# Performance work log

Measured on AMD Instinct MI355X. Metric: run time of the kernel, lower is better.

The kernel has to match this reference:

```python
import jax, jax.numpy as jnp
import numpy as np

B, T, D, H = 4, 4096, 1024, 16
HD = D // H  # head_dim = 64


def setup_inputs() -> dict:
    key = jax.random.key(0)
    k1, k2, k3 = jax.random.split(key, 3)
    x = jax.random.normal(k1, (B, T, D), dtype=jnp.float32)
    # torch Linear weight is (out,in); we store transposed (in,out) for x @ W
    Wqkv = jax.random.normal(k2, (D, 3 * D), dtype=jnp.float32) * 0.02
    Wout = jax.random.normal(k3, (D, D), dtype=jnp.float32) * 0.02
    return {"x": x, "Wqkv": Wqkv, "Wout": Wout}


def reference(x, Wqkv, Wout):
    # Faithful to original: qkv reshaped to (B,T,3,H,hd) WITHOUT moving heads to
    # a batch dim, so attention mixes the H heads of each token (scores: B,T,H,H).
    qkv = (x @ Wqkv).reshape(B, T, 3, H, HD)
    q, k, v = qkv[:, :, 0], qkv[:, :, 1], qkv[:, :, 2]  # each (B,T,H,HD)
    scores = jnp.einsum('btid,btjd->btij', q, k) / jnp.sqrt(jnp.float32(HD))
    attn = jax.nn.softmax(scores, axis=-1)  # softmax over heads j
    out = jnp.einsum('btij,btjd->btid', attn, v).reshape(B, T, D)
    return out @ Wout
```

## Files before the change

### kernel.cpp

```cpp
#include <hip/hip_runtime.h>
#include <hip/hip_bf16.h>
#include <cstdint>
#include <cstddef>


typedef __bf16 bf16x8 __attribute__((ext_vector_type(8)));
typedef __bf16 bf16x4 __attribute__((ext_vector_type(4)));
typedef float  f32x4  __attribute__((ext_vector_type(4)));

#define AS1 __attribute__((address_space(1)))
#define AS3 __attribute__((address_space(3)))

__device__ __forceinline__ void async_copy16(const void* g, void* l) {
    __builtin_amdgcn_global_load_lds((const AS1 void*)g, (AS3 void*)l, 16, 0, 0);
}

__global__ __launch_bounds__(256) void cvt_bf16_kernel(const float4* __restrict__ in,
                                                       bf16x4* __restrict__ out, int n4) {
    int i = blockIdx.x * 256 + threadIdx.x;
    if (i >= n4) return;
    float4 v = in[i];
    bf16x4 o = { (__bf16)v.x, (__bf16)v.y, (__bf16)v.z, (__bf16)v.w };
    out[i] = o;
}

__global__ __launch_bounds__(256) void transpose_cvt_kernel(const float* __restrict__ in,
                                                            __bf16* __restrict__ out,
                                                            int R, int C) {
    __shared__ float tile[32][33];
    int c0 = blockIdx.x * 32, r0 = blockIdx.y * 32;
    int tx = threadIdx.x, ty = threadIdx.y;
    #pragma unroll
    for (int i = 0; i < 32; i += 8)
        tile[ty + i][tx] = in[(size_t)(r0 + ty + i) * C + c0 + tx];
    __syncthreads();
    #pragma unroll
    for (int i = 0; i < 32; i += 8)
        out[(size_t)(c0 + ty + i) * R + r0 + tx] = (__bf16)tile[tx][ty + i];
}

template<int OUT_BF16>
__global__ __launch_bounds__(256) void gemm_bt(const __bf16* __restrict__ A,
                                               const __bf16* __restrict__ Bt,
                                               void* __restrict__ Cv,
                                               int N, int K) {
    __shared__ __bf16 As[128 * 32];
    __shared__ __bf16 Bs[128 * 32];

    const int tid  = threadIdx.x;
    const int wave = tid >> 6;
    const int lane = tid & 63;
    const int quad = lane >> 4;
    const int q16  = lane & 15;
    const int wr   = wave >> 1, wc = wave & 1;
    const int row0 = blockIdx.y * 128;
    const int col0 = blockIdx.x * 128;

    const __bf16* Ag = A  + (size_t)row0 * K;
    const __bf16* Bg = Bt + (size_t)col0 * K;

    const int o0 = (wave * 2)     * 1024 + lane * 16;
    const int o1 = (wave * 2 + 1) * 1024 + lane * 16;
    const int r0 = o0 >> 6, r1 = o1 >> 6;
    const int cb0 = ((o0 >> 4) & 3) ^ ((r0 >> 1) & 3);
    const int cb1 = ((o1 >> 4) & 3) ^ ((r1 >> 1) & 3);
    char* ldsA0 = (char*)As + (wave * 2)     * 1024;
    char* ldsA1 = (char*)As + (wave * 2 + 1) * 1024;
    char* ldsB0 = (char*)Bs + (wave * 2)     * 1024;
    char* ldsB1 = (char*)Bs + (wave * 2 + 1) * 1024;

    f32x4 acc[4][4] = {};

    for (int k0 = 0; k0 < K; k0 += 32) {
        async_copy16(Ag + (size_t)r0 * K + (k0 + cb0 * 8), ldsA0);
        async_copy16(Ag + (size_t)r1 * K + (k0 + cb1 * 8), ldsA1);
        async_copy16(Bg + (size_t)r0 * K + (k0 + cb0 * 8), ldsB0);
        async_copy16(Bg + (size_t)r1 * K + (k0 + cb1 * 8), ldsB1);
        __syncthreads();

        bf16x8 af[4], bfr[4];
        #pragma unroll
        for (int mi = 0; mi < 4; ++mi) {
            int row = wr * 64 + mi * 16 + q16;
            int sl  = quad ^ ((row >> 1) & 3);
            af[mi] = *(const bf16x8*)((const char*)As + row * 64 + sl * 16);
        }
        #pragma unroll
        for (int ni = 0; ni < 4; ++ni) {
            int row = wc * 64 + ni * 16 + q16;
            int sl  = quad ^ ((row >> 1) & 3);
            bfr[ni] = *(const bf16x8*)((const char*)Bs + row * 64 + sl * 16);
        }
        #pragma unroll
        for (int mi = 0; mi < 4; ++mi)
            #pragma unroll
            for (int ni = 0; ni < 4; ++ni)
                acc[mi][ni] = __builtin_amdgcn_mfma_f32_16x16x32_bf16(af[mi], bfr[ni], acc[mi][ni], 0, 0, 0);
        __syncthreads();
    }

    #pragma unroll
    for (int mi = 0; mi < 4; ++mi) {
        #pragma unroll
        for (int ni = 0; ni < 4; ++ni) {
            int col = col0 + wc * 64 + ni * 16 + q16;
            #pragma unroll
            for (int r = 0; r < 4; ++r) {
                int row = row0 + wr * 64 + mi * 16 + quad * 4 + r;
                if (OUT_BF16)
                    ((__bf16*)Cv)[(size_t)row * N + col] = (__bf16)acc[mi][ni][r];
                else
                    ((float*)Cv)[(size_t)row * N + col] = acc[mi][ni][r];
            }
        }
    }
}

__global__ __launch_bounds__(256) void attn_mfma_kernel(const __bf16* __restrict__ qkv,
                                                        __bf16* __restrict__ ao) {
    const int tok  = blockIdx.x * 4 + (threadIdx.x >> 6);
    const int lane = threadIdx.x & 63;
    const int quad = lane >> 4;
    const int q16  = lane & 15;

    const __bf16* base = qkv + (size_t)tok * 3072;
    const __bf16* vb   = base + 2048;

    const bf16x8 qf0 = *(const bf16x8*)(base + q16 * 64 + quad * 8);
    const bf16x8 qf1 = *(const bf16x8*)(base + q16 * 64 + quad * 8 + 32);
    const bf16x8 kf0 = *(const bf16x8*)(base + 1024 + q16 * 64 + quad * 8);
    const bf16x8 kf1 = *(const bf16x8*)(base + 1024 + q16 * 64 + quad * 8 + 32);

    f32x4 st = {0.f, 0.f, 0.f, 0.f};
    st = __builtin_amdgcn_mfma_f32_16x16x32_bf16(kf0, qf0, st, 0, 0, 0);
    st = __builtin_amdgcn_mfma_f32_16x16x32_bf16(kf1, qf1, st, 0, 0, 0);

    float s0 = st[0] * 0.125f, s1 = st[1] * 0.125f, s2 = st[2] * 0.125f, s3 = st[3] * 0.125f;
    float m = fmaxf(fmaxf(s0, s1), fmaxf(s2, s3));
    m = fmaxf(m, __shfl_xor(m, 16));
    m = fmaxf(m, __shfl_xor(m, 32));
    float e0 = __expf(s0 - m), e1 = __expf(s1 - m), e2 = __expf(s2 - m), e3 = __expf(s3 - m);
    float sum = e0 + e1 + e2 + e3;
    sum += __shfl_xor(sum, 16);
    sum += __shfl_xor(sum, 32);
    const float inv = 1.f / sum;

    union { __bf16 h[2]; int i; } u01, u23;
    u01.h[0] = (__bf16)(e0 * inv); u01.h[1] = (__bf16)(e1 * inv);
    u23.h[0] = (__bf16)(e2 * inv); u23.h[1] = (__bf16)(e3 * inv);

    const int src0 = quad * 32 + q16;
    const int src1 = src0 + 16;
    union { int i[4]; bf16x8 v; } af;
    af.i[0] = __shfl(u01.i, src0);
    af.i[1] = __shfl(u23.i, src0);
    af.i[2] = __shfl(u01.i, src1);
    af.i[3] = __shfl(u23.i, src1);
    if (quad >= 2) { af.i[0] = 0; af.i[1] = 0; af.i[2] = 0; af.i[3] = 0; }

    __bf16* outp = ao + (size_t)tok * 1024;
    #pragma unroll
    for (int c = 0; c < 4; ++c) {
        const int d0 = c * 16;
        bf16x8 bf = {};
        if (quad < 2) {
            #pragma unroll
            for (int idx = 0; idx < 8; ++idx)
                bf[idx] = vb[(quad * 8 + idx) * 64 + d0 + q16];
        }
        f32x4 acc = {0.f, 0.f, 0.f, 0.f};
        acc = __builtin_amdgcn_mfma_f32_16x16x32_bf16(af.v, bf, acc, 0, 0, 0);
        #pragma unroll
        for (int r = 0; r < 4; ++r)
            outp[(quad * 4 + r) * 64 + d0 + q16] = (__bf16)acc[r];
    }
}

extern "C" void kernel_launch(void* const* d_in, const int* in_sizes, int n_in,
                              void* d_out, int out_size, void* d_ws, size_t ws_size,
                              hipStream_t stream) {
    const float* x    = (const float*)d_in[0];
    const float* Wqkv = (const float*)d_in[1];
    const float* Wout = (const float*)d_in[2];
    float* out = (float*)d_out;

    char* ws = (char*)d_ws;
    __bf16* xb    = (__bf16*)(ws);
    __bf16* wqkvT = (__bf16*)(ws + 33554432);
    __bf16* woutT = (__bf16*)(ws + 33554432 + 6291456);
    __bf16* qkv   = (__bf16*)(ws + 33554432 + 6291456 + 2097152);
    __bf16* ao    = (__bf16*)(ws + 33554432 + 6291456 + 2097152 + 100663296);

    cvt_bf16_kernel<<<16384, 256, 0, stream>>>((const float4*)x, (bf16x4*)xb, 4194304);
    transpose_cvt_kernel<<<dim3(96, 32), dim3(32, 8), 0, stream>>>(Wqkv, wqkvT, 1024, 3072);
    transpose_cvt_kernel<<<dim3(32, 32), dim3(32, 8), 0, stream>>>(Wout, woutT, 1024, 1024);
    gemm_bt<1><<<dim3(24, 128), 256, 0, stream>>>(xb, wqkvT, (void*)qkv, 3072, 1024);
    attn_mfma_kernel<<<4096, 256, 0, stream>>>(qkv, ao);
    gemm_bt<0><<<dim3(8, 128), 256, 0, stream>>>(ao, woutT, (void*)out, 1024, 1024);
}
```

Before: 350.4 us.

## Permute weight columns so attention loads and stores are contiguous vectors

The transpose kernels now permute the output columns of Wqkv and the input rows of Wout, so the QKV GEMM writes q/k/v in the exact per-lane fragment order the attention MFMAs consume. The attention output is written in a permuted order that the permuted Wout rows undo. This turns strided scalar V gathers and scattered 2-byte output stores into 16-byte vector loads and stores. The attention kernel is a small part of the total compared with the two GEMMs, and the weight preprocessing gains index arithmetic and less coalesced scattered writes.

Result: no change. 350.3 us (-0.0%).

```diff
diff --git a/kernel.cpp b/kernel.cpp
--- a/kernel.cpp
+++ b/kernel.cpp
@@ -13,6 +13,17 @@
 
 __device__ __forceinline__ void async_copy16(const void* g, void* l) {
     __builtin_amdgcn_global_load_lds((const AS1 void*)g, (AS3 void*)l, 16, 0, 0);
+}
+
+__device__ __forceinline__ int invp_qkv(int col) {
+    int g = col >> 10;
+    if (g == 2) { int q = col & 1023; return 2048 + ((q & 63) << 4) + (q >> 6); }
+    int h = (col >> 6) & 15, d = col & 63;
+    return (g << 10) + ((d & 32) << 4) + (((d >> 3) & 3) << 7) + (h << 3) + (d & 7);
+}
+
+__device__ __forceinline__ int invp_ao(int k) {
+    return (((k >> 8) & 3) << 8) + ((k & 15) << 4) + (((k >> 4) & 3) << 2) + ((k >> 6) & 3);
 }
 
 __global__ __launch_bounds__(256) void cvt_bf16_kernel(const float4* __restrict__ in,
@@ -24,10 +35,10 @@
     out[i] = o;
 }
 
-__global__ __launch_bounds__(256) void transpose_cvt_kernel(const float* __restrict__ in,
-                                                            __bf16* __restrict__ out,
-                                                            int R, int C) {
+__global__ __launch_bounds__(256) void transpose_qkv_kernel(const float* __restrict__ in,
+                                                            __bf16* __restrict__ out) {
     __shared__ float tile[32][33];
+    const int C = 3072;
     int c0 = blockIdx.x * 32, r0 = blockIdx.y * 32;
     int tx = threadIdx.x, ty = threadIdx.y;
     #pragma unroll
@@ -35,8 +46,26 @@
         tile[ty + i][tx] = in[(size_t)(r0 + ty + i) * C + c0 + tx];
     __syncthreads();
     #pragma unroll
+    for (int i = 0; i < 32; i += 8) {
+        int prow = invp_qkv(c0 + ty + i);
+        out[(size_t)prow * 1024 + r0 + tx] = (__bf16)tile[tx][ty + i];
+    }
+}
+
+__global__ __launch_bounds__(256) void transpose_wout_kernel(const float* __restrict__ in,
+                                                             __bf16* __restrict__ out) {
+    __shared__ float tile[32][33];
+    const int C = 1024;
+    int c0 = blockIdx.x * 32, r0 = blockIdx.y * 32;
+    int tx = threadIdx.x, ty = threadIdx.y;
+    #pragma unroll
     for (int i = 0; i < 32; i += 8)
-        out[(size_t)(c0 + ty + i) * R + r0 + tx] = (__bf16)tile[tx][ty + i];
+        tile[ty + i][tx] = in[(size_t)(r0 + ty + i) * C + c0 + tx];
+    __syncthreads();
+    int pk = invp_ao(r0 + tx);
+    #pragma unroll
+    for (int i = 0; i < 32; i += 8)
+        out[(size_t)(c0 + ty + i) * 1024 + pk] = (__bf16)tile[tx][ty + i];
 }
 
 template<int OUT_BF16>
@@ -124,12 +153,11 @@
     const int q16  = lane & 15;
 
     const __bf16* base = qkv + (size_t)tok * 3072;
-    const __bf16* vb   = base + 2048;
-
-    const bf16x8 qf0 = *(const bf16x8*)(base + q16 * 64 + quad * 8);
-    const bf16x8 qf1 = *(const bf16x8*)(base + q16 * 64 + quad * 8 + 32);
-    const bf16x8 kf0 = *(const bf16x8*)(base + 1024 + q16 * 64 + quad * 8);
-    const bf16x8 kf1 = *(const bf16x8*)(base + 1024 + q16 * 64 + quad * 8 + 32);
+
+    const bf16x8 qf0 = *(const bf16x8*)(base + lane * 8);
+    const bf16x8 qf1 = *(const bf16x8*)(base + 512 + lane * 8);
+    const bf16x8 kf0 = *(const bf16x8*)(base + 1024 + lane * 8);
+    const bf16x8 kf1 = *(const bf16x8*)(base + 1536 + lane * 8);
 
     f32x4 st = {0.f, 0.f, 0.f, 0.f};
     st = __builtin_amdgcn_mfma_f32_16x16x32_bf16(kf0, qf0, st, 0, 0, 0);
@@ -158,22 +186,26 @@
     af.i[3] = __shfl(u23.i, src1);
     if (quad >= 2) { af.i[0] = 0; af.i[1] = 0; af.i[2] = 0; af.i[3] = 0; }
 
-    __bf16* outp = ao + (size_t)tok * 1024;
+    const __bf16* vb = base + 2048;
+    f32x4 accs[4];
     #pragma unroll
     for (int c = 0; c < 4; ++c) {
-        const int d0 = c * 16;
-        bf16x8 bf = {};
-        if (quad < 2) {
-            #pragma unroll
-            for (int idx = 0; idx < 8; ++idx)
-                bf[idx] = vb[(quad * 8 + idx) * 64 + d0 + q16];
-        }
-        f32x4 acc = {0.f, 0.f, 0.f, 0.f};
-        acc = __builtin_amdgcn_mfma_f32_16x16x32_bf16(af.v, bf, acc, 0, 0, 0);
+        bf16x8 bfv = {};
+        if (quad < 2)
+            bfv = *(const bf16x8*)(vb + (c * 16 + q16) * 16 + quad * 8);
+        f32x4 z = {0.f, 0.f, 0.f, 0.f};
+        accs[c] = __builtin_amdgcn_mfma_f32_16x16x32_bf16(af.v, bfv, z, 0, 0, 0);
+    }
+
+    union { __bf16 h[16]; bf16x8 v[2]; } o;
+    #pragma unroll
+    for (int c = 0; c < 4; ++c)
         #pragma unroll
         for (int r = 0; r < 4; ++r)
-            outp[(quad * 4 + r) * 64 + d0 + q16] = (__bf16)acc[r];
-    }
+            o.h[c * 4 + r] = (__bf16)accs[c][r];
+    __bf16* outp = ao + (size_t)tok * 1024 + lane * 16;
+    *(bf16x8*)outp = o.v[0];
+    *(bf16x8*)(outp + 8) = o.v[1];
 }
 
 extern "C" void kernel_launch(void* const* d_in, const int* in_sizes, int n_in,
@@ -192,8 +224,8 @@
     __bf16* ao    = (__bf16*)(ws + 33554432 + 6291456 + 2097152 + 100663296);
 
     cvt_bf16_kernel<<<16384, 256, 0, stream>>>((const float4*)x, (bf16x4*)xb, 4194304);
-    transpose_cvt_kernel<<<dim3(96, 32), dim3(32, 8), 0, stream>>>(Wqkv, wqkvT, 1024, 3072);
-    transpose_cvt_kernel<<<dim3(32, 32), dim3(32, 8), 0, stream>>>(Wout, woutT, 1024, 1024);
+    transpose_qkv_kernel<<<dim3(96, 32), dim3(32, 8), 0, stream>>>(Wqkv, wqkvT);
+    transpose_wout_kernel<<<dim3(32, 32), dim3(32, 8), 0, stream>>>(Wout, woutT);
     gemm_bt<1><<<dim3(24, 128), 256, 0, stream>>>(xb, wqkvT, (void*)qkv, 3072, 1024);
     attn_mfma_kernel<<<4096, 256, 0, stream>>>(qkv, ao);
     gemm_bt<0><<<dim3(8, 128), 256, 0, stream>>>(ao, woutT, (void*)out, 1024, 1024);
```
